# Kernel optimization log

Measured on AMD Instinct MI355X. Metric: run time of the kernel, lower is better.

Reference implementation:

```python
import jax, jax.numpy as jnp
import numpy as np
import math

N_NODES = 100000
N_EDGES = 3200000
NFEAT = 512
NHID = 256
NCLASS = 16
NLAYERS = 8
LAMDA = 0.5
ALPHA = 0.1


def setup_inputs() -> dict:
    key = jax.random.key(0)
    ks = jax.random.split(key, 10)
    x = jax.random.normal(ks[0], (N_NODES, NFEAT), dtype=jnp.float32)
    edge_src = jax.random.randint(ks[1], (N_EDGES,), 0, N_NODES, dtype=jnp.int32)
    edge_dst = jax.random.randint(ks[2], (N_EDGES,), 0, N_NODES, dtype=jnp.int32)
    edge_w = jax.random.uniform(ks[3], (N_EDGES,), dtype=jnp.float32)
    # fcs[0]: Linear(nfeat, nhidden); fcs[1]: Linear(nhidden, nclass)
    s0 = 1.0 / math.sqrt(NFEAT)
    w0 = jax.random.uniform(ks[4], (NFEAT, NHID), minval=-s0, maxval=s0, dtype=jnp.float32)
    b0 = jax.random.uniform(ks[5], (NHID,), minval=-s0, maxval=s0, dtype=jnp.float32)
    # conv weights: uniform(-1/sqrt(out_features), +), out_features = nhidden
    sc = 1.0 / math.sqrt(NHID)
    conv_w = jax.random.uniform(ks[6], (NLAYERS, NHID, NHID), minval=-sc, maxval=sc, dtype=jnp.float32)
    w1 = jax.random.uniform(ks[7], (NHID, NCLASS), minval=-sc, maxval=sc, dtype=jnp.float32)
    b1 = jax.random.uniform(ks[8], (NCLASS,), minval=-sc, maxval=sc, dtype=jnp.float32)
    return {"x": x, "edge_src": edge_src, "edge_dst": edge_dst, "edge_w": edge_w,
            "w0": w0, "b0": b0, "conv_w": conv_w, "w1": w1, "b1": b1}


def _spmm(edge_src, edge_dst, edge_w, h):
    # torch.spmm(adj, h): out[i] = sum_j adj[i,j] * h[j], adj in COO (dst=row, src=col)
    msgs = edge_w[:, None] * h[edge_src]            # [E, H] irregular gather
    return jax.ops.segment_sum(msgs, edge_dst, num_segments=h.shape[0])


def reference(x, edge_src, edge_dst, edge_w, w0, b0, conv_w, w1, b1):
    # eval mode: F.dropout is identity
    h = jax.nn.relu(x @ w0 + b0)                    # [N, NHID]
    h0 = h
    for i in range(NLAYERS):
        theta = math.log(LAMDA / (i + 1) + 1.0)
        hi = _spmm(edge_src, edge_dst, edge_w, h)   # sparse aggregate
        support = (1.0 - ALPHA) * hi + ALPHA * h0   # initial residual (GCNII)
        out = theta * (support @ conv_w[i]) + (1.0 - theta) * support
        h = jax.nn.relu(out + h)                    # layer residual
    return jax.nn.sigmoid(h @ w1 + b1)              # [N, NCLASS]
```

## Files before the change

kernel.cpp:

```cpp
#include <hip/hip_runtime.h>
#include <math.h>

#define N_NODES 100000
#define N_EDGES 3200000
#define NFEAT 512
#define NHID 256
#define NCLASS 16
#define NLAYERS 8

#define SCAN_CHUNK 1024
#define NB ((N_NODES + SCAN_CHUNK - 1) / SCAN_CHUNK)

__global__ void k_hist(const int* __restrict__ dst, int* __restrict__ cnt) {
  int i = blockIdx.x * 256 + threadIdx.x;
  if (i < N_EDGES) atomicAdd(&cnt[dst[i]], 1);
}

__global__ void k_blocksum(const int* __restrict__ cnt, int* __restrict__ bs) {
  __shared__ int red[256];
  int b = blockIdx.x, t = threadIdx.x;
  int s = 0;
  int base = b * SCAN_CHUNK;
  for (int j = 0; j < 4; ++j) {
    int i = base + t + j * 256;
    if (i < N_NODES) s += cnt[i];
  }
  red[t] = s;
  __syncthreads();
  for (int off = 128; off > 0; off >>= 1) {
    if (t < off) red[t] += red[t + off];
    __syncthreads();
  }
  if (t == 0) bs[b] = red[0];
}

__global__ void k_scan_top(int* __restrict__ bs, int* __restrict__ rp) {
  if (threadIdx.x == 0) {
    int run = 0;
    for (int b = 0; b < NB; ++b) { int v = bs[b]; bs[b] = run; run += v; }
    rp[N_NODES] = run;
  }
}

__global__ void k_scan_write(const int* __restrict__ cnt, const int* __restrict__ bs,
                             int* __restrict__ rp) {
  __shared__ int tot[256];
  int b = blockIdx.x, t = threadIdx.x;
  int base = b * SCAN_CHUNK + t * 4;
  int v0 = 0, v1 = 0, v2 = 0, v3 = 0;
  if (base + 0 < N_NODES) v0 = cnt[base + 0];
  if (base + 1 < N_NODES) v1 = cnt[base + 1];
  if (base + 2 < N_NODES) v2 = cnt[base + 2];
  if (base + 3 < N_NODES) v3 = cnt[base + 3];
  int tsum = v0 + v1 + v2 + v3;
  tot[t] = tsum;
  __syncthreads();
  for (int off = 1; off < 256; off <<= 1) {
    int v = 0;
    if (t >= off) v = tot[t - off];
    __syncthreads();
    if (t >= off) tot[t] += v;
    __syncthreads();
  }
  int excl = tot[t] - tsum + bs[b];
  if (base + 0 < N_NODES) rp[base + 0] = excl;
  if (base + 1 < N_NODES) rp[base + 1] = excl + v0;
  if (base + 2 < N_NODES) rp[base + 2] = excl + v0 + v1;
  if (base + 3 < N_NODES) rp[base + 3] = excl + v0 + v1 + v2;
}

__global__ void k_fill(const int* __restrict__ src, const int* __restrict__ dst,
                       const float* __restrict__ w, const int* __restrict__ rp,
                       int* __restrict__ fill, int* __restrict__ col,
                       float* __restrict__ val) {
  int i = blockIdx.x * 256 + threadIdx.x;
  if (i < N_EDGES) {
    int d = dst[i];
    int pos = rp[d] + atomicAdd(&fill[d], 1);
    col[pos] = src[i];
    val[pos] = w[i];
  }
}

__global__ __launch_bounds__(256)
void k_spmm_half(const int* __restrict__ rp, const int* __restrict__ col,
                 const float* __restrict__ val, const float* __restrict__ h,
                 const float* __restrict__ h0, float* __restrict__ sup, int f0) {
  int wave = threadIdx.x >> 6;
  int lane = threadIdx.x & 63;
  int node = blockIdx.x * 4 + wave;
  if (node >= N_NODES) return;
  int e0 = rp[node], e1 = rp[node + 1];
  const float2* __restrict__ hv = (const float2*)h;
  int fo = (f0 >> 1) + lane;

  float2 a0 = make_float2(0.f, 0.f);
  float2 a1 = make_float2(0.f, 0.f);
  float2 a2 = make_float2(0.f, 0.f);
  float2 a3 = make_float2(0.f, 0.f);

  int e = e0;
  for (; e + 4 <= e1; e += 4) {
    int s0 = col[e], s1 = col[e + 1], s2 = col[e + 2], s3 = col[e + 3];
    float w0 = val[e], w1 = val[e + 1], w2 = val[e + 2], w3 = val[e + 3];
    float2 v0 = hv[(size_t)s0 * 128 + fo];
    float2 v1 = hv[(size_t)s1 * 128 + fo];
    float2 v2 = hv[(size_t)s2 * 128 + fo];
    float2 v3 = hv[(size_t)s3 * 128 + fo];
    a0.x += w0 * v0.x; a0.y += w0 * v0.y;
    a1.x += w1 * v1.x; a1.y += w1 * v1.y;
    a2.x += w2 * v2.x; a2.y += w2 * v2.y;
    a3.x += w3 * v3.x; a3.y += w3 * v3.y;
  }
  for (; e < e1; ++e) {
    int s0 = col[e];
    float w0 = val[e];
    float2 v0 = hv[(size_t)s0 * 128 + fo];
    a0.x += w0 * v0.x; a0.y += w0 * v0.y;
  }

  float2 acc;
  acc.x = (a0.x + a1.x) + (a2.x + a3.x);
  acc.y = (a0.y + a1.y) + (a2.y + a3.y);

  float2 z = ((const float2*)h0)[(size_t)node * 128 + fo];
  float2 o;
  o.x = 0.9f * acc.x + 0.1f * z.x;
  o.y = 0.9f * acc.y + 0.1f * z.y;
  ((float2*)sup)[(size_t)node * 128 + fo] = o;
}

template <int MODE>
__global__ __launch_bounds__(256)
void k_gemm(const float* __restrict__ A, const float* __restrict__ W, int K,
            const float* __restrict__ bias, const float* __restrict__ hin,
            float* __restrict__ out1, float* __restrict__ out2, float theta) {
  __shared__ float As[16][128];
  __shared__ float Bs[16][128];
  int bm = blockIdx.x * 128, bn = blockIdx.y * 128;
  int tid = threadIdx.x;
  int tx = tid & 15, ty = tid >> 4;
  float acc[8][8];
#pragma unroll
  for (int i = 0; i < 8; ++i)
#pragma unroll
    for (int j = 0; j < 8; ++j) acc[i][j] = 0.f;

  for (int kc = 0; kc < K; kc += 16) {
#pragma unroll
    for (int it = 0; it < 2; ++it) {
      int idx = tid + it * 256;
      int m = idx >> 2, q = (idx & 3) * 4;
      int gm = bm + m;
      float4 f = make_float4(0.f, 0.f, 0.f, 0.f);
      if (gm < N_NODES) f = *(const float4*)&A[(size_t)gm * K + kc + q];
      As[q + 0][m] = f.x; As[q + 1][m] = f.y; As[q + 2][m] = f.z; As[q + 3][m] = f.w;
    }
#pragma unroll
    for (int it = 0; it < 2; ++it) {
      int idx = tid + it * 256;
      int kk = idx >> 5, nq = (idx & 31) * 4;
      *(float4*)&Bs[kk][nq] = *(const float4*)&W[(size_t)(kc + kk) * NHID + bn + nq];
    }
    __syncthreads();
#pragma unroll
    for (int k = 0; k < 16; ++k) {
      float a[8], b[8];
      *(float4*)&a[0] = *(const float4*)&As[k][ty * 8];
      *(float4*)&a[4] = *(const float4*)&As[k][ty * 8 + 4];
      *(float4*)&b[0] = *(const float4*)&Bs[k][tx * 4];
      *(float4*)&b[4] = *(const float4*)&Bs[k][tx * 4 + 64];
#pragma unroll
      for (int i = 0; i < 8; ++i)
#pragma unroll
        for (int j = 0; j < 8; ++j) acc[i][j] += a[i] * b[j];
    }
    __syncthreads();
  }

  int c0 = bn + tx * 4, c1 = bn + 64 + tx * 4;
#pragma unroll
  for (int i = 0; i < 8; ++i) {
    int gm = bm + ty * 8 + i;
    if (gm >= N_NODES) continue;
    size_t r0 = (size_t)gm * NHID + c0;
    size_t r1 = (size_t)gm * NHID + c1;
    if (MODE == 0) {
      float4 bb0 = *(const float4*)&bias[c0];
      float4 bb1 = *(const float4*)&bias[c1];
      float4 o0, o1;
      o0.x = fmaxf(acc[i][0] + bb0.x, 0.f);
      o0.y = fmaxf(acc[i][1] + bb0.y, 0.f);
      o0.z = fmaxf(acc[i][2] + bb0.z, 0.f);
      o0.w = fmaxf(acc[i][3] + bb0.w, 0.f);
      o1.x = fmaxf(acc[i][4] + bb1.x, 0.f);
      o1.y = fmaxf(acc[i][5] + bb1.y, 0.f);
      o1.z = fmaxf(acc[i][6] + bb1.z, 0.f);
      o1.w = fmaxf(acc[i][7] + bb1.w, 0.f);
      *(float4*)&out1[r0] = o0;
      *(float4*)&out1[r1] = o1;
      *(float4*)&out2[r0] = o0;
      *(float4*)&out2[r1] = o1;
    } else {
      float omt = 1.f - theta;
      float4 s0 = *(const float4*)&A[r0];
      float4 s1 = *(const float4*)&A[r1];
      float4 h0v = *(const float4*)&hin[r0];
      float4 h1v = *(const float4*)&hin[r1];
      float4 o0, o1;
      o0.x = fmaxf(theta * acc[i][0] + omt * s0.x + h0v.x, 0.f);
      o0.y = fmaxf(theta * acc[i][1] + omt * s0.y + h0v.y, 0.f);
      o0.z = fmaxf(theta * acc[i][2] + omt * s0.z + h0v.z, 0.f);
      o0.w = fmaxf(theta * acc[i][3] + omt * s0.w + h0v.w, 0.f);
      o1.x = fmaxf(theta * acc[i][4] + omt * s1.x + h1v.x, 0.f);
      o1.y = fmaxf(theta * acc[i][5] + omt * s1.y + h1v.y, 0.f);
      o1.z = fmaxf(theta * acc[i][6] + omt * s1.z + h1v.z, 0.f);
      o1.w = fmaxf(theta * acc[i][7] + omt * s1.w + h1v.w, 0.f);
      *(float4*)&out1[r0] = o0;
      *(float4*)&out1[r1] = o1;
    }
  }
}

__global__ __launch_bounds__(256)
void k_final(const float* __restrict__ h, const float* __restrict__ w1,
             const float* __restrict__ b1, float* __restrict__ out) {
  __shared__ float ws[NHID * NCLASS];
  int t = threadIdx.x;
  for (int i = t; i < NHID * NCLASS; i += 256) ws[i] = w1[i];
  __syncthreads();
  int node = blockIdx.x * 16 + (t >> 4);
  int c = t & 15;
  if (node >= N_NODES) return;
  float acc = b1[c];
  const float* hr = &h[(size_t)node * NHID];
  for (int k = 0; k < NHID; k += 4) {
    float4 hv = *(const float4*)&hr[k];
    acc += hv.x * ws[(k + 0) * NCLASS + c];
    acc += hv.y * ws[(k + 1) * NCLASS + c];
    acc += hv.z * ws[(k + 2) * NCLASS + c];
    acc += hv.w * ws[(k + 3) * NCLASS + c];
  }
  out[(size_t)node * NCLASS + c] = 1.f / (1.f + __expf(-acc));
}

extern "C" void kernel_launch(void* const* d_in, const int* in_sizes, int n_in,
                              void* d_out, int out_size, void* d_ws, size_t ws_size,
                              hipStream_t stream) {
  const float* x        = (const float*)d_in[0];
  const int*   edge_src = (const int*)d_in[1];
  const int*   edge_dst = (const int*)d_in[2];
  const float* edge_w   = (const float*)d_in[3];
  const float* w0       = (const float*)d_in[4];
  const float* b0       = (const float*)d_in[5];
  const float* conv_w   = (const float*)d_in[6];
  const float* w1       = (const float*)d_in[7];
  const float* b1       = (const float*)d_in[8];
  float* out = (float*)d_out;

  char* ws = (char*)d_ws;
  size_t off = 0;
  auto alloc = [&](size_t bytes) {
    size_t o = off;
    off = (off + bytes + 255) & ~(size_t)255;
    return (void*)(ws + o);
  };
  float* h   = (float*)alloc((size_t)N_NODES * NHID * 4);
  float* h0  = (float*)alloc((size_t)N_NODES * NHID * 4);
  float* sup = (float*)alloc((size_t)N_NODES * NHID * 4);
  int*   rp  = (int*)alloc((size_t)(N_NODES + 1) * 4);
  int*   cnt = (int*)alloc((size_t)N_NODES * 4);
  int*   col = (int*)alloc((size_t)N_EDGES * 4);
  float* val = (float*)alloc((size_t)N_EDGES * 4);
  int*   bs  = (int*)alloc((size_t)NB * 4);
  (void)ws_size;

  hipMemsetAsync(cnt, 0, (size_t)N_NODES * 4, stream);
  k_hist<<<(N_EDGES + 255) / 256, 256, 0, stream>>>(edge_dst, cnt);
  k_blocksum<<<NB, 256, 0, stream>>>(cnt, bs);
  k_scan_top<<<1, 64, 0, stream>>>(bs, rp);
  k_scan_write<<<NB, 256, 0, stream>>>(cnt, bs, rp);
  hipMemsetAsync(cnt, 0, (size_t)N_NODES * 4, stream);
  k_fill<<<(N_EDGES + 255) / 256, 256, 0, stream>>>(edge_src, edge_dst, edge_w, rp,
                                                    cnt, col, val);

  dim3 g0((N_NODES + 127) / 128, NHID / 128);
  k_gemm<0><<<g0, 256, 0, stream>>>(x, w0, NFEAT, b0, nullptr, h, h0, 0.f);

  for (int i = 0; i < NLAYERS; ++i) {
    float theta = logf(0.5f / (float)(i + 1) + 1.0f);
    k_spmm_half<<<(N_NODES + 3) / 4, 256, 0, stream>>>(rp, col, val, h, h0, sup, 0);
    k_spmm_half<<<(N_NODES + 3) / 4, 256, 0, stream>>>(rp, col, val, h, h0, sup, 128);
    const float* cw = conv_w + (size_t)i * NHID * NHID;
    k_gemm<1><<<g0, 256, 0, stream>>>(sup, cw, NHID, nullptr, h, h, nullptr, theta);
  }

  k_final<<<(N_NODES + 15) / 16, 256, 0, stream>>>(h, w1, b1, out);
}
```

Before: 5.956 ms.

## Restructure GEMM with register prefetch, direct weight loads, and single h0 write

```diff
diff --git a/kernel.cpp b/kernel.cpp
--- a/kernel.cpp
+++ b/kernel.cpp
@@ -130,55 +130,74 @@
   ((float2*)sup)[(size_t)node * 128 + fo] = o;
 }
 
-template <int MODE>
-__global__ __launch_bounds__(256)
-void k_gemm(const float* __restrict__ A, const float* __restrict__ W, int K,
-            const float* __restrict__ bias, const float* __restrict__ hin,
-            float* __restrict__ out1, float* __restrict__ out2, float theta) {
-  __shared__ float As[16][128];
-  __shared__ float Bs[16][128];
+template <int K, int MODE>
+__global__ __launch_bounds__(256, 4)
+void k_gemm2(const float* __restrict__ A, const float* __restrict__ W,
+             const float* __restrict__ bias, const float* __restrict__ hin,
+             float* __restrict__ out1, float theta) {
+  __shared__ float As[32][132];
+  constexpr int NCHUNK = K / 32;
   int bm = blockIdx.x * 128, bn = blockIdx.y * 128;
   int tid = threadIdx.x;
   int tx = tid & 15, ty = tid >> 4;
+  int c0 = bn + tx * 4, c1 = bn + 64 + tx * 4;
+
   float acc[8][8];
 #pragma unroll
   for (int i = 0; i < 8; ++i)
 #pragma unroll
     for (int j = 0; j < 8; ++j) acc[i][j] = 0.f;
 
-  for (int kc = 0; kc < K; kc += 16) {
-#pragma unroll
-    for (int it = 0; it < 2; ++it) {
-      int idx = tid + it * 256;
-      int m = idx >> 2, q = (idx & 3) * 4;
-      int gm = bm + m;
-      float4 f = make_float4(0.f, 0.f, 0.f, 0.f);
-      if (gm < N_NODES) f = *(const float4*)&A[(size_t)gm * K + kc + q];
-      As[q + 0][m] = f.x; As[q + 1][m] = f.y; As[q + 2][m] = f.z; As[q + 3][m] = f.w;
+  float4 pf[4];
+#pragma unroll
+  for (int j = 0; j < 4; ++j) {
+    int idx = tid + j * 256;
+    int m = idx >> 3, q = (idx & 7) * 4;
+    int gm = bm + m;
+    pf[j] = make_float4(0.f, 0.f, 0.f, 0.f);
+    if (gm < N_NODES) pf[j] = *(const float4*)&A[(size_t)gm * K + q];
+  }
+
+  for (int c = 0; c < NCHUNK; ++c) {
+    __syncthreads();
+#pragma unroll
+    for (int j = 0; j < 4; ++j) {
+      int idx = tid + j * 256;
+      int m = idx >> 3, q = (idx & 7) * 4;
+      As[q + 0][m] = pf[j].x;
+      As[q + 1][m] = pf[j].y;
+      As[q + 2][m] = pf[j].z;
+      As[q + 3][m] = pf[j].w;
     }
-#pragma unroll
-    for (int it = 0; it < 2; ++it) {
-      int idx = tid + it * 256;
-      int kk = idx >> 5, nq = (idx & 31) * 4;
-      *(float4*)&Bs[kk][nq] = *(const float4*)&W[(size_t)(kc + kk) * NHID + bn + nq];
+    __syncthreads();
+
+    if (c + 1 < NCHUNK) {
+      int kc = (c + 1) * 32;
+#pragma unroll
+      for (int j = 0; j < 4; ++j) {
+        int idx = tid + j * 256;
+        int m = idx >> 3, q = (idx & 7) * 4;
+        int gm = bm + m;
+        pf[j] = make_float4(0.f, 0.f, 0.f, 0.f);
+        if (gm < N_NODES) pf[j] = *(const float4*)&A[(size_t)gm * K + kc + q];
+      }
     }
-    __syncthreads();
-#pragma unroll
-    for (int k = 0; k < 16; ++k) {
+
+    const float* __restrict__ Wc = W + (size_t)(c * 32) * NHID;
+#pragma unroll
+    for (int k = 0; k < 32; ++k) {
       float a[8], b[8];
       *(float4*)&a[0] = *(const float4*)&As[k][ty * 8];
       *(float4*)&a[4] = *(const float4*)&As[k][ty * 8 + 4];
-      *(float4*)&b[0] = *(const float4*)&Bs[k][tx * 4];
-      *(float4*)&b[4] = *(const float4*)&Bs[k][tx * 4 + 64];
+      *(float4*)&b[0] = *(const float4*)&Wc[(size_t)k * NHID + c0];
+      *(float4*)&b[4] = *(const float4*)&Wc[(size_t)k * NHID + c1];
 #pragma unroll
       for (int i = 0; i < 8; ++i)
 #pragma unroll
         for (int j = 0; j < 8; ++j) acc[i][j] += a[i] * b[j];
     }
-    __syncthreads();
-  }
-
-  int c0 = bn + tx * 4, c1 = bn + 64 + tx * 4;
+  }
+
 #pragma unroll
   for (int i = 0; i < 8; ++i) {
     int gm = bm + ty * 8 + i;
@@ -199,8 +218,6 @@
       o1.w = fmaxf(acc[i][7] + bb1.w, 0.f);
       *(float4*)&out1[r0] = o0;
       *(float4*)&out1[r1] = o1;
-      *(float4*)&out2[r0] = o0;
-      *(float4*)&out2[r1] = o1;
     } else {
       float omt = 1.f - theta;
       float4 s0 = *(const float4*)&A[r0];
@@ -285,14 +302,15 @@
                                                     cnt, col, val);
 
   dim3 g0((N_NODES + 127) / 128, NHID / 128);
-  k_gemm<0><<<g0, 256, 0, stream>>>(x, w0, NFEAT, b0, nullptr, h, h0, 0.f);
+  k_gemm2<NFEAT, 0><<<g0, 256, 0, stream>>>(x, w0, b0, nullptr, h0, 0.f);
 
   for (int i = 0; i < NLAYERS; ++i) {
     float theta = logf(0.5f / (float)(i + 1) + 1.0f);
-    k_spmm_half<<<(N_NODES + 3) / 4, 256, 0, stream>>>(rp, col, val, h, h0, sup, 0);
-    k_spmm_half<<<(N_NODES + 3) / 4, 256, 0, stream>>>(rp, col, val, h, h0, sup, 128);
+    const float* hcur = (i == 0) ? h0 : h;
+    k_spmm_half<<<(N_NODES + 3) / 4, 256, 0, stream>>>(rp, col, val, hcur, h0, sup, 0);
+    k_spmm_half<<<(N_NODES + 3) / 4, 256, 0, stream>>>(rp, col, val, hcur, h0, sup, 128);
     const float* cw = conv_w + (size_t)i * NHID * NHID;
-    k_gemm<1><<<g0, 256, 0, stream>>>(sup, cw, NHID, nullptr, h, h, nullptr, theta);
+    k_gemm2<NHID, 1><<<g0, 256, 0, stream>>>(sup, cw, nullptr, hcur, h, theta);
   }
 
   k_final<<<(N_NODES + 15) / 16, 256, 0, stream>>>(h, w1, b1, out);
```

Measured after the change: 9.788 ms. 64.3% more time.
